# Performance work log

Measured on AMD Instinct MI355X. Metric: run time of the kernel, lower is better.

## Reference

```python
import jax, jax.numpy as jnp
import numpy as np

DIM = 1024
NH = 16
HD = DIM // NH
EPS = 1e-5


def setup_inputs() -> dict:
    key = jax.random.key(0)
    ks = jax.random.split(key, 6)
    B, LQ, LK = 8, 512, 1024
    s = 1.0 / np.sqrt(DIM)
    return {
        "text_tokens": jax.random.normal(ks[0], (B, LQ, DIM), dtype=jnp.float32),
        "vision_tokens": jax.random.normal(ks[1], (B, LK, DIM), dtype=jnp.float32),
        "in_proj_w": jax.random.normal(ks[2], (3 * DIM, DIM), dtype=jnp.float32) * s,
        "in_proj_b": jnp.zeros((3 * DIM,), dtype=jnp.float32),
        "out_w": jax.random.normal(ks[3], (DIM, DIM), dtype=jnp.float32) * s,
        "out_b": jnp.zeros((DIM,), dtype=jnp.float32),
        "ln_g": jnp.ones((DIM,), dtype=jnp.float32),
        "ln_b": jnp.zeros((DIM,), dtype=jnp.float32),
    }


def _layernorm(x, g, b):
    mu = jnp.mean(x, axis=-1, keepdims=True)
    var = jnp.mean(jnp.square(x - mu), axis=-1, keepdims=True)
    return (x - mu) * jax.lax.rsqrt(var + EPS) * g + b


def reference(text_tokens, vision_tokens, in_proj_w, in_proj_b, out_w, out_b, ln_g, ln_b):
    B, LQ, _ = text_tokens.shape
    LK = vision_tokens.shape[1]
    wq, wk, wv = in_proj_w[:DIM], in_proj_w[DIM:2 * DIM], in_proj_w[2 * DIM:]
    bq, bk, bv = in_proj_b[:DIM], in_proj_b[DIM:2 * DIM], in_proj_b[2 * DIM:]
    q = (text_tokens @ wq.T + bq).reshape(B, LQ, NH, HD)
    k = (vision_tokens @ wk.T + bk).reshape(B, LK, NH, HD)
    v = (vision_tokens @ wv.T + bv).reshape(B, LK, NH, HD)
    scale = 1.0 / np.sqrt(HD)
    scores = jnp.einsum("bqhd,bkhd->bhqk", q, k) * scale  # [B,H,LQ,LK]
    probs = jax.nn.softmax(scores, axis=-1)
    ctx = jnp.einsum("bhqk,bkhd->bqhd", probs, v).reshape(B, LQ, DIM)
    attended = ctx @ out_w.T + out_b
    out = _layernorm(attended + text_tokens, ln_g, ln_b)
    attn_weights = jnp.mean(probs, axis=1)  # PyTorch average_attn_weights=True
    return out, attn_weights
```

## Files before the change

### kernel.cpp

```cpp
#include <hip/hip_runtime.h>

#define DIMV 1024
#define NHV  16
#define HDV  64
#define BV   8
#define LQV  512
#define LKV  1024
#define PSTR 1032

typedef __bf16 bfrag  __attribute__((ext_vector_type(8)));
typedef float  f32x4  __attribute__((ext_vector_type(4)));
typedef unsigned short u16;
typedef unsigned int   u32;
typedef unsigned long long u64;

typedef const __attribute__((address_space(1))) u32 gu32;
typedef __attribute__((address_space(3))) u32 lu32;

__device__ __forceinline__ u16 f2bf(float f) {
    u32 x = __builtin_bit_cast(u32, f);
    x = x + 0x7FFFu + ((x >> 16) & 1u);
    return (u16)(x >> 16);
}

__device__ __forceinline__ void g2l16(const u16* g, const u16* l) {
    __builtin_amdgcn_global_load_lds(
        reinterpret_cast<gu32*>(reinterpret_cast<u64>(g)),
        reinterpret_cast<lu32*>((u32)reinterpret_cast<u64>(l)),
        16, 0, 0);
}

__global__ __launch_bounds__(256)
void cast_all(const float* __restrict__ vis,  const float* __restrict__ wqkv,
              const float* __restrict__ outw, const float* __restrict__ text,
              u16* __restrict__ vis_bf, u16* __restrict__ wqkv_bf,
              u16* __restrict__ outw_bf, u16* __restrict__ text_bf)
{
    const int bx = blockIdx.x;
    const float* src; u16* dst; int i;
    if (bx < 8192)       { src = vis;  dst = vis_bf;  i = bx * 256 + threadIdx.x; }
    else if (bx < 11264) { src = wqkv; dst = wqkv_bf; i = (bx - 8192) * 256 + threadIdx.x; }
    else if (bx < 12288) { src = outw; dst = outw_bf; i = (bx - 11264) * 256 + threadIdx.x; }
    else                 { src = text; dst = text_bf; i = (bx - 12288) * 256 + threadIdx.x; }
    const float4 v = reinterpret_cast<const float4*>(src)[i];
    ushort4 o;
    o.x = f2bf(v.x); o.y = f2bf(v.y); o.z = f2bf(v.z); o.w = f2bf(v.w);
    reinterpret_cast<ushort4*>(dst)[i] = o;
}

__global__ __launch_bounds__(256)
void qkv_gemm(const u16* __restrict__ text_bf, const u16* __restrict__ vis_bf,
              const u16* __restrict__ wqkv_bf, const float* __restrict__ bqkv,
              u16* __restrict__ qb, u16* __restrict__ kb, u16* __restrict__ vTb)
{
    __shared__ __align__(16) u16 sA[128 * 64];
    __shared__ __align__(16) u16 sB[128 * 64];

    const int bx = blockIdx.x;
    const u16* A; const u16* W; const float* bias; u16* C; int mb, vmode;
    if (bx < 32)      { A = text_bf; W = wqkv_bf;               bias = bqkv;        C = qb;  mb = bx * 128;        vmode = 0; }
    else if (bx < 96) { A = vis_bf;  W = wqkv_bf + 1024 * 1024; bias = bqkv + 1024; C = kb;  mb = (bx - 32) * 128; vmode = 0; }
    else              { A = vis_bf;  W = wqkv_bf + 2097152;     bias = bqkv + 2048; C = vTb; mb = (bx - 96) * 128; vmode = 1; }

    const int t    = threadIdx.x;
    const int lane = t & 63;
    const int w    = t >> 6;
    const int quad = lane >> 4;
    const int r    = lane & 15;
    const int wr   = (w >> 1) * 64;
    const int wc   = (w & 1) * 64;
    const int nb   = blockIdx.y * 128;

    const int srow  = lane >> 3;
    const int skoff = (lane & 7) * 8;

    f32x4 acc[4][4] = {};

    const u16* Abase = A + (size_t)mb * 1024 + skoff;
    const u16* Wbase = W + (size_t)nb * 1024 + skoff;

    for (int k0 = 0; k0 < 1024; k0 += 64) {
#pragma unroll
        for (int it = 0; it < 4; ++it) {
            const int c = w * 4 + it;
            const int row = c * 8 + srow;
            g2l16(Abase + (size_t)row * 1024 + k0, sA + c * 512);
            g2l16(Wbase + (size_t)row * 1024 + k0, sB + c * 512);
        }
        __syncthreads();
#pragma unroll
        for (int kk = 0; kk < 2; ++kk) {
            bfrag af[4], bg[4];
#pragma unroll
            for (int i = 0; i < 4; ++i)
                af[i] = *reinterpret_cast<const bfrag*>(sA + (wr + i * 16 + r) * 64 + kk * 32 + quad * 8);
#pragma unroll
            for (int j = 0; j < 4; ++j)
                bg[j] = *reinterpret_cast<const bfrag*>(sB + (wc + j * 16 + r) * 64 + kk * 32 + quad * 8);
#pragma unroll
            for (int i = 0; i < 4; ++i)
#pragma unroll
                for (int j = 0; j < 4; ++j)
                    acc[i][j] = __builtin_amdgcn_mfma_f32_16x16x32_bf16(af[i], bg[j], acc[i][j], 0, 0, 0);
        }
        __syncthreads();
    }

#pragma unroll
    for (int i = 0; i < 4; i++)
#pragma unroll
    for (int j = 0; j < 4; j++) {
        const int colg = nb + wc + j * 16 + r;
        const float bv = bias[colg];
#pragma unroll
        for (int reg = 0; reg < 4; reg++) {
            const int rowg = mb + wr + i * 16 + quad * 4 + reg;
            const float v = acc[i][j][reg] + bv;
            if (vmode == 0) {
                C[(size_t)rowg * 1024 + colg] = f2bf(v);
            } else {
                C[((size_t)((rowg >> 10) << 10) + colg) * 1024 + (rowg & 1023)] = f2bf(v);
            }
        }
    }
}

__global__ __launch_bounds__(256)
void gemm_out(const u16* __restrict__ A, const u16* __restrict__ W,
              const float* __restrict__ bias, float* __restrict__ Cout,
              const float* __restrict__ resid)
{
    __shared__ __align__(16) u16 sA[128 * 64];
    __shared__ __align__(16) u16 sB[128 * 64];

    const int t    = threadIdx.x;
    const int lane = t & 63;
    const int w    = t >> 6;
    const int quad = lane >> 4;
    const int r    = lane & 15;
    const int wr   = (w >> 1) * 64;
    const int wc   = (w & 1) * 64;
    const int mb   = blockIdx.x * 128;
    const int nb   = blockIdx.y * 128;

    const int srow  = lane >> 3;
    const int skoff = (lane & 7) * 8;

    f32x4 acc[4][4] = {};

    const u16* Abase = A + (size_t)mb * 1024 + skoff;
    const u16* Wbase = W + (size_t)nb * 1024 + skoff;

    for (int k0 = 0; k0 < 1024; k0 += 64) {
#pragma unroll
        for (int it = 0; it < 4; ++it) {
            const int c = w * 4 + it;
            const int row = c * 8 + srow;
            g2l16(Abase + (size_t)row * 1024 + k0, sA + c * 512);
            g2l16(Wbase + (size_t)row * 1024 + k0, sB + c * 512);
        }
        __syncthreads();
#pragma unroll
        for (int kk = 0; kk < 2; ++kk) {
            bfrag af[4], bg[4];
#pragma unroll
            for (int i = 0; i < 4; ++i)
                af[i] = *reinterpret_cast<const bfrag*>(sA + (wr + i * 16 + r) * 64 + kk * 32 + quad * 8);
#pragma unroll
            for (int j = 0; j < 4; ++j)
                bg[j] = *reinterpret_cast<const bfrag*>(sB + (wc + j * 16 + r) * 64 + kk * 32 + quad * 8);
#pragma unroll
            for (int i = 0; i < 4; ++i)
#pragma unroll
                for (int j = 0; j < 4; ++j)
                    acc[i][j] = __builtin_amdgcn_mfma_f32_16x16x32_bf16(af[i], bg[j], acc[i][j], 0, 0, 0);
        }
        __syncthreads();
    }

#pragma unroll
    for (int i = 0; i < 4; i++)
#pragma unroll
    for (int j = 0; j < 4; j++) {
        const int colg = nb + wc + j * 16 + r;
        const float bv = bias[colg];
#pragma unroll
        for (int reg = 0; reg < 4; reg++) {
            const int rowg = mb + wr + i * 16 + quad * 4 + reg;
            const float v = acc[i][j][reg] + bv;
            Cout[(size_t)rowg * 1024 + colg] = v + resid[(size_t)rowg * 1024 + colg];
        }
    }
}

__global__ __launch_bounds__(512, 2)
void attn_kernel(const u16* __restrict__ q, const u16* __restrict__ k,
                 const u16* __restrict__ vT, u16* __restrict__ ctx,
                 float* __restrict__ attnw)
{
    __shared__ __align__(16) u16 sP[2][2][16 * PSTR];
    __shared__ float reds[2][2][64];

    const int t    = threadIdx.x;
    const int g    = t >> 8;
    const int tg   = t & 255;
    const int lane = tg & 63;
    const int w    = tg >> 6;
    const int quad = lane >> 4;
    const int r    = lane & 15;
    const int b    = blockIdx.x;
    const int q0   = blockIdx.y * 16;

    const int row16 = quad * 4;
    const float scale = 0.125f;

    f32x4 wacc[16] = {};

    for (int hh = 0; hh < 8; ++hh) {
        const int h = g * 8 + hh;
        const int p = hh & 1;
        const int dbase = h * HDV + quad * 8;

        const u16* qp = q + (size_t)(b * LQV + q0 + r) * DIMV + dbase;
        const bfrag qa0 = *reinterpret_cast<const bfrag*>(qp);
        const bfrag qa1 = *reinterpret_cast<const bfrag*>(qp + 32);

        f32x4 s[16];
#pragma unroll
        for (int i = 0; i < 16; ++i) {
            const int n0 = w * 256 + i * 16;
            const u16* kp = k + (size_t)(b * LKV + n0 + r) * DIMV + dbase;
            const bfrag kb0 = *reinterpret_cast<const bfrag*>(kp);
            const bfrag kb1 = *reinterpret_cast<const bfrag*>(kp + 32);
            f32x4 a = {};
            a    = __builtin_amdgcn_mfma_f32_16x16x32_bf16(qa0, kb0, a, 0, 0, 0);
            s[i] = __builtin_amdgcn_mfma_f32_16x16x32_bf16(qa1, kb1, a, 0, 0, 0);
        }

        float sw[4] = {0.f, 0.f, 0.f, 0.f};
#pragma unroll
        for (int i = 0; i < 16; ++i)
#pragma unroll
            for (int reg = 0; reg < 4; ++reg) {
                s[i][reg] = __expf(s[i][reg] * scale);
                sw[reg] += s[i][reg];
            }
#pragma unroll
        for (int reg = 0; reg < 4; ++reg)
#pragma unroll
            for (int off = 1; off < 16; off <<= 1)
                sw[reg] += __shfl_xor(sw[reg], off);

        if (r == 0) {
#pragma unroll
            for (int reg = 0; reg < 4; ++reg)
                reds[g][p][w * 16 + row16 + reg] = sw[reg];
        }

#pragma unroll
        for (int i = 0; i < 16; ++i)
#pragma unroll
            for (int reg = 0; reg < 4; ++reg)
                sP[g][p][(row16 + reg) * PSTR + w * 256 + i * 16 + r] = f2bf(s[i][reg]);

        __syncthreads();

        float factor[4];
#pragma unroll
        for (int reg = 0; reg < 4; ++reg) {
            const int rr = row16 + reg;
            const float tot = reds[g][p][rr]      + reds[g][p][16 + rr] +
                              reds[g][p][32 + rr] + reds[g][p][48 + rr];
            factor[reg] = 1.0f / tot;
        }

#pragma unroll
        for (int i = 0; i < 16; ++i)
#pragma unroll
            for (int reg = 0; reg < 4; ++reg)
                wacc[i][reg] += s[i][reg] * factor[reg];

        {
            const int n0 = w * 16;
            f32x4 c0 = {}, c1 = {}, c2 = {}, c3 = {};
            const u16* vb = vT + (size_t)(b * DIMV + h * HDV + n0 + r) * LKV;
            const u16* sPb = &sP[g][p][r * PSTR + quad * 8];
#pragma unroll
            for (int kk = 0; kk < LKV; kk += 128) {
                const bfrag a0 = *reinterpret_cast<const bfrag*>(sPb + kk);
                const bfrag a1 = *reinterpret_cast<const bfrag*>(sPb + kk + 32);
                const bfrag a2 = *reinterpret_cast<const bfrag*>(sPb + kk + 64);
                const bfrag a3 = *reinterpret_cast<const bfrag*>(sPb + kk + 96);
                const bfrag b0 = *reinterpret_cast<const bfrag*>(vb + kk      + quad * 8);
                const bfrag b1 = *reinterpret_cast<const bfrag*>(vb + kk + 32 + quad * 8);
                const bfrag b2 = *reinterpret_cast<const bfrag*>(vb + kk + 64 + quad * 8);
                const bfrag b3 = *reinterpret_cast<const bfrag*>(vb + kk + 96 + quad * 8);
                c0 = __builtin_amdgcn_mfma_f32_16x16x32_bf16(a0, b0, c0, 0, 0, 0);
                c1 = __builtin_amdgcn_mfma_f32_16x16x32_bf16(a1, b1, c1, 0, 0, 0);
                c2 = __builtin_amdgcn_mfma_f32_16x16x32_bf16(a2, b2, c2, 0, 0, 0);
                c3 = __builtin_amdgcn_mfma_f32_16x16x32_bf16(a3, b3, c3, 0, 0, 0);
            }
            const f32x4 c = (c0 + c1) + (c2 + c3);
#pragma unroll
            for (int reg = 0; reg < 4; ++reg)
                ctx[(size_t)(b * LQV + q0 + row16 + reg) * DIMV + h * HDV + n0 + r] =
                    f2bf(c[reg] * factor[reg]);
        }
    }

    __syncthreads();

    float* cb = reinterpret_cast<float*>(&sP[0][0][0]);
    if (g == 1) {
#pragma unroll
        for (int i = 0; i < 16; ++i)
#pragma unroll
            for (int reg = 0; reg < 4; ++reg)
                cb[(i * 4 + reg) * 256 + tg] = wacc[i][reg];
    }
    __syncthreads();
    if (g == 0) {
        const float inv16 = 1.0f / 16.0f;
#pragma unroll
        for (int i = 0; i < 16; ++i)
#pragma unroll
            for (int reg = 0; reg < 4; ++reg) {
                const float v = (wacc[i][reg] + cb[(i * 4 + reg) * 256 + tg]) * inv16;
                attnw[(size_t)(b * LQV + q0 + row16 + reg) * LKV + w * 256 + i * 16 + r] = v;
            }
    }
}

__global__ __launch_bounds__(256)
void ln_kernel(const float* __restrict__ x, const float* __restrict__ g,
               const float* __restrict__ bta, float* __restrict__ out)
{
    __shared__ float red[8];
    const int row = blockIdx.x;
    const int t = threadIdx.x;
    const int w = t >> 6;
    const float4 xv = reinterpret_cast<const float4*>(x + (size_t)row * DIMV)[t];

    float s = xv.x + xv.y + xv.z + xv.w;
#pragma unroll
    for (int off = 32; off; off >>= 1) s += __shfl_down(s, off);
    if ((t & 63) == 0) red[w] = s;
    __syncthreads();
    const float mu = (red[0] + red[1] + red[2] + red[3]) * (1.0f / 1024.0f);

    const float d0 = xv.x - mu, d1 = xv.y - mu, d2 = xv.z - mu, d3 = xv.w - mu;
    float s2 = d0 * d0 + d1 * d1 + d2 * d2 + d3 * d3;
#pragma unroll
    for (int off = 32; off; off >>= 1) s2 += __shfl_down(s2, off);
    if ((t & 63) == 0) red[4 + w] = s2;
    __syncthreads();
    const float var = (red[4] + red[5] + red[6] + red[7]) * (1.0f / 1024.0f);
    const float inv = rsqrtf(var + 1e-5f);

    float4 o;
    const int c = t * 4;
    o.x = d0 * inv * g[c + 0] + bta[c + 0];
    o.y = d1 * inv * g[c + 1] + bta[c + 1];
    o.z = d2 * inv * g[c + 2] + bta[c + 2];
    o.w = d3 * inv * g[c + 3] + bta[c + 3];
    reinterpret_cast<float4*>(out + (size_t)row * DIMV)[t] = o;
}

extern "C" void kernel_launch(void* const* d_in, const int* in_sizes, int n_in,
                              void* d_out, int out_size, void* d_ws, size_t ws_size,
                              hipStream_t stream)
{
    const float* text = (const float*)d_in[0];
    const float* vis  = (const float*)d_in[1];
    const float* wqkv = (const float*)d_in[2];
    const float* bqkv = (const float*)d_in[3];
    const float* outw = (const float*)d_in[4];
    const float* outb = (const float*)d_in[5];
    const float* lng  = (const float*)d_in[6];
    const float* lnb  = (const float*)d_in[7];

    char* ws = (char*)d_ws;
    u16*   vis_bf  = (u16*)(ws);
    u16*   ctxb    = (u16*)(ws);
    u16*   wqkv_bf = (u16*)(ws + (size_t)(16u << 20));
    u16*   outw_bf = (u16*)(ws + (size_t)(22u << 20));
    u16*   qb      = (u16*)(ws + (size_t)(24u << 20));
    u16*   kb      = (u16*)(ws + (size_t)(32u << 20));
    float* attb    = (float*)(ws + (size_t)(32u << 20));
    u16*   vTb     = (u16*)(ws + (size_t)(48u << 20));

    float* outp  = (float*)d_out;
    float* attnw = outp + (size_t)4096 * 1024;
    u16*   text_bf = (u16*)outp;

    const dim3 blk(256);
    cast_all<<<dim3(16384), blk, 0, stream>>>(vis, wqkv, outw, text,
                                              vis_bf, wqkv_bf, outw_bf, text_bf);
    qkv_gemm<<<dim3(160, 8), blk, 0, stream>>>(text_bf, vis_bf, wqkv_bf, bqkv, qb, kb, vTb);
    attn_kernel<<<dim3(8, 32), dim3(512), 0, stream>>>(qb, kb, vTb, ctxb, attnw);
    gemm_out<<<dim3(32, 8), blk, 0, stream>>>(ctxb, outw_bf, outb, attb, text);
    ln_kernel<<<dim3(4096), blk, 0, stream>>>(attb, lng, lnb, outp);
}
```

Measured before the change: 374.0 us.

## Chunk QK scores, accumulate head-mean from shared bf16 probs with row-contiguous ownership

The score tile is now computed in chunks of four MFMA results, each immediately exponentiated and written to shared memory, so the sixteen score registers no longer stay live. The head-averaged attention-weight accumulator is rebuilt from the shared bf16 probabilities of both head groups, with each thread owning 32 contiguous columns of one row. That removes the final cross-group shared-memory reduction and its two barriers, and lets the attnw output go out as float4 stores. The PV MFMA loop is also wrapped in s_setprio. The trade-off is that the averaged weights now come from bf16-rounded probabilities, which adds some error, and there are extra LDS reads every head.

Result: no change. 377.1 us (+0.8%).

```diff
diff --git a/kernel.cpp b/kernel.cpp
--- a/kernel.cpp
+++ b/kernel.cpp
@@ -13,6 +13,7 @@
 typedef unsigned short u16;
 typedef unsigned int   u32;
 typedef unsigned long long u64;
+typedef u16 u16x8 __attribute__((ext_vector_type(8)));
 
 typedef const __attribute__((address_space(1))) u32 gu32;
 typedef __attribute__((address_space(3))) u32 lu32;
@@ -21,6 +22,11 @@
     u32 x = __builtin_bit_cast(u32, f);
     x = x + 0x7FFFu + ((x >> 16) & 1u);
     return (u16)(x >> 16);
+}
+
+__device__ __forceinline__ float b2f(u16 v) {
+    u32 x = ((u32)v) << 16;
+    return __builtin_bit_cast(float, x);
 }
 
 __device__ __forceinline__ void g2l16(const u16* g, const u16* l) {
@@ -214,7 +220,10 @@
     const int row16 = quad * 4;
     const float scale = 0.125f;
 
-    f32x4 wacc[16] = {};
+    const int arow = t & 15;
+    const int ac0  = (t >> 4) * 32;
+
+    float wacc[32] = {};
 
     for (int hh = 0; hh < 8; ++hh) {
         const int h = g * 8 + hh;
@@ -225,66 +234,74 @@
         const bfrag qa0 = *reinterpret_cast<const bfrag*>(qp);
         const bfrag qa1 = *reinterpret_cast<const bfrag*>(qp + 32);
 
-        f32x4 s[16];
-#pragma unroll
-        for (int i = 0; i < 16; ++i) {
-            const int n0 = w * 256 + i * 16;
-            const u16* kp = k + (size_t)(b * LKV + n0 + r) * DIMV + dbase;
-            const bfrag kb0 = *reinterpret_cast<const bfrag*>(kp);
-            const bfrag kb1 = *reinterpret_cast<const bfrag*>(kp + 32);
-            f32x4 a = {};
-            a    = __builtin_amdgcn_mfma_f32_16x16x32_bf16(qa0, kb0, a, 0, 0, 0);
-            s[i] = __builtin_amdgcn_mfma_f32_16x16x32_bf16(qa1, kb1, a, 0, 0, 0);
-        }
-
         float sw[4] = {0.f, 0.f, 0.f, 0.f};
 #pragma unroll
-        for (int i = 0; i < 16; ++i)
-#pragma unroll
-            for (int reg = 0; reg < 4; ++reg) {
-                s[i][reg] = __expf(s[i][reg] * scale);
-                sw[reg] += s[i][reg];
+        for (int ch = 0; ch < 4; ++ch) {
+            f32x4 s4[4];
+#pragma unroll
+            for (int u = 0; u < 4; ++u) {
+                const int i = ch * 4 + u;
+                const u16* kp = k + (size_t)(b * LKV + w * 256 + i * 16 + r) * DIMV + dbase;
+                const bfrag kb0 = *reinterpret_cast<const bfrag*>(kp);
+                const bfrag kb1 = *reinterpret_cast<const bfrag*>(kp + 32);
+                f32x4 a = {};
+                a     = __builtin_amdgcn_mfma_f32_16x16x32_bf16(qa0, kb0, a, 0, 0, 0);
+                s4[u] = __builtin_amdgcn_mfma_f32_16x16x32_bf16(qa1, kb1, a, 0, 0, 0);
             }
+#pragma unroll
+            for (int u = 0; u < 4; ++u) {
+                const int i = ch * 4 + u;
+#pragma unroll
+                for (int reg = 0; reg < 4; ++reg) {
+                    const float e = __expf(s4[u][reg] * scale);
+                    sw[reg] += e;
+                    sP[g][p][(row16 + reg) * PSTR + w * 256 + i * 16 + r] = f2bf(e);
+                }
+            }
+        }
+
 #pragma unroll
         for (int reg = 0; reg < 4; ++reg)
 #pragma unroll
             for (int off = 1; off < 16; off <<= 1)
                 sw[reg] += __shfl_xor(sw[reg], off);
-
         if (r == 0) {
 #pragma unroll
             for (int reg = 0; reg < 4; ++reg)
                 reds[g][p][w * 16 + row16 + reg] = sw[reg];
         }
 
-#pragma unroll
-        for (int i = 0; i < 16; ++i)
-#pragma unroll
-            for (int reg = 0; reg < 4; ++reg)
-                sP[g][p][(row16 + reg) * PSTR + w * 256 + i * 16 + r] = f2bf(s[i][reg]);
-
         __syncthreads();
 
         float factor[4];
 #pragma unroll
         for (int reg = 0; reg < 4; ++reg) {
             const int rr = row16 + reg;
-            const float tot = reds[g][p][rr]      + reds[g][p][16 + rr] +
-                              reds[g][p][32 + rr] + reds[g][p][48 + rr];
-            factor[reg] = 1.0f / tot;
-        }
-
-#pragma unroll
-        for (int i = 0; i < 16; ++i)
-#pragma unroll
-            for (int reg = 0; reg < 4; ++reg)
-                wacc[i][reg] += s[i][reg] * factor[reg];
+            factor[reg] = 1.0f / (reds[g][p][rr]      + reds[g][p][16 + rr] +
+                                  reds[g][p][32 + rr] + reds[g][p][48 + rr]);
+        }
+
+        {
+            const float f0 = 1.0f / (reds[0][p][arow]      + reds[0][p][16 + arow] +
+                                     reds[0][p][32 + arow] + reds[0][p][48 + arow]);
+            const float f1 = 1.0f / (reds[1][p][arow]      + reds[1][p][16 + arow] +
+                                     reds[1][p][32 + arow] + reds[1][p][48 + arow]);
+#pragma unroll
+            for (int m = 0; m < 4; ++m) {
+                const u16x8 p0 = *reinterpret_cast<const u16x8*>(&sP[0][p][arow * PSTR + ac0 + m * 8]);
+                const u16x8 p1 = *reinterpret_cast<const u16x8*>(&sP[1][p][arow * PSTR + ac0 + m * 8]);
+#pragma unroll
+                for (int e = 0; e < 8; ++e)
+                    wacc[m * 8 + e] += b2f(p0[e]) * f0 + b2f(p1[e]) * f1;
+            }
+        }
 
         {
             const int n0 = w * 16;
             f32x4 c0 = {}, c1 = {}, c2 = {}, c3 = {};
             const u16* vb = vT + (size_t)(b * DIMV + h * HDV + n0 + r) * LKV;
             const u16* sPb = &sP[g][p][r * PSTR + quad * 8];
+            __builtin_amdgcn_s_setprio(1);
 #pragma unroll
             for (int kk = 0; kk < LKV; kk += 128) {
                 const bfrag a0 = *reinterpret_cast<const bfrag*>(sPb + kk);
@@ -300,6 +317,7 @@
                 c2 = __builtin_amdgcn_mfma_f32_16x16x32_bf16(a2, b2, c2, 0, 0, 0);
                 c3 = __builtin_amdgcn_mfma_f32_16x16x32_bf16(a3, b3, c3, 0, 0, 0);
             }
+            __builtin_amdgcn_s_setprio(0);
             const f32x4 c = (c0 + c1) + (c2 + c3);
 #pragma unroll
             for (int reg = 0; reg < 4; ++reg)
@@ -308,26 +326,18 @@
         }
     }
 
-    __syncthreads();
-
-    float* cb = reinterpret_cast<float*>(&sP[0][0][0]);
-    if (g == 1) {
-#pragma unroll
-        for (int i = 0; i < 16; ++i)
-#pragma unroll
-            for (int reg = 0; reg < 4; ++reg)
-                cb[(i * 4 + reg) * 256 + tg] = wacc[i][reg];
-    }
-    __syncthreads();
-    if (g == 0) {
+    {
         const float inv16 = 1.0f / 16.0f;
-#pragma unroll
-        for (int i = 0; i < 16; ++i)
-#pragma unroll
-            for (int reg = 0; reg < 4; ++reg) {
-                const float v = (wacc[i][reg] + cb[(i * 4 + reg) * 256 + tg]) * inv16;
-                attnw[(size_t)(b * LQV + q0 + row16 + reg) * LKV + w * 256 + i * 16 + r] = v;
-            }
+        float* ap = attnw + (size_t)(b * LQV + q0 + arow) * LKV + ac0;
+#pragma unroll
+        for (int j = 0; j < 32; j += 4) {
+            float4 o;
+            o.x = wacc[j]     * inv16;
+            o.y = wacc[j + 1] * inv16;
+            o.z = wacc[j + 2] * inv16;
+            o.w = wacc[j + 3] * inv16;
+            *reinterpret_cast<float4*>(ap + j) = o;
+        }
     }
 }
 
```
